# Performance work log

Hardware: AMD Instinct MI355X
Metric: run time of the kernel (lower is better)

## Reference

```python
import jax, jax.numpy as jnp
import numpy as np

B, S, D = 4, 2048, 768
H = 12
DH = D // H  # 64


def setup_inputs() -> dict:
    key = jax.random.key(0)
    ks = jax.random.split(key, 6)
    scale = 0.02
    return {
        "hidden_states": jax.random.normal(ks[0], (B, S, D), dtype=jnp.float32),
        "Wq": jax.random.normal(ks[1], (D, D), dtype=jnp.float32) * scale,
        "bq": jnp.zeros((D,), dtype=jnp.float32),
        "Wk": jax.random.normal(ks[2], (D, D), dtype=jnp.float32) * scale,
        "bk": jnp.zeros((D,), dtype=jnp.float32),
        "Wv": jax.random.normal(ks[3], (D, D), dtype=jnp.float32) * scale,
        "bv": jnp.zeros((D,), dtype=jnp.float32),
        "Wo": jax.random.normal(ks[4], (D, D), dtype=jnp.float32) * scale,
        "bo": jnp.zeros((D,), dtype=jnp.float32),
        "w_mix": jnp.ones((2,), dtype=jnp.float32),
    }


def reference(hidden_states, Wq, bq, Wk, bk, Wv, bv, Wo, bo, w_mix):
    # Q/K/V projections, then split heads: [B,S,D] -> [B,H,S,DH]
    def split_heads(x):
        return x.reshape(B, S, H, DH).transpose(0, 2, 1, 3)

    q = split_heads(hidden_states @ Wq.T + bq)
    k = split_heads(hidden_states @ Wk.T + bk)
    v = split_heads(hidden_states @ Wv.T + bv)

    # [B,H,S,S] attention scores
    scores = jnp.einsum("bhqd,bhkd->bhqk", q, k) / jnp.sqrt(jnp.float32(DH))

    attn_soft = jax.nn.softmax(scores, axis=-1)
    attn_relu2 = jnp.square(jax.nn.relu(scores))
    mix = jax.nn.softmax(w_mix)  # exp(w)/sum(exp(w))
    attn = attn_soft * mix[0] + attn_relu2 * mix[1]
    # dropout rate 0.0 (inference) -> identity

    ctx = jnp.einsum("bhqk,bhkd->bhqd", attn, v)
    ctx = ctx.transpose(0, 2, 1, 3).reshape(B, S, D)
    out = ctx @ Wo.T + bo
    return out
```

## Files before the change

kernel.cpp:

```cpp
#include <hip/hip_runtime.h>

#define DEV __device__ __forceinline__

typedef __attribute__((ext_vector_type(8))) short short8;
typedef __attribute__((ext_vector_type(4))) float f32x4;
typedef __attribute__((ext_vector_type(2))) unsigned int u32x2;
typedef __attribute__((ext_vector_type(4))) unsigned int u32x4;

constexpr int Dm = 768;
constexpr int Sn = 2048;
constexpr int Bn = 4;
constexpr int Hn = 12;
constexpr int Mn = Bn * Sn;

constexpr float kQScale = 0.18033688011112043f;
constexpr float kR2Fix  = 0.4804530139182014f;

DEV unsigned short f32_to_bf16(float f) {
  unsigned int u = __float_as_uint(f);
  u = (u + 0x7fffu + ((u >> 16) & 1u)) >> 16;
  return (unsigned short)u;
}

DEV unsigned cvt_pk_bf16(float lo, float hi) {
  unsigned d;
  asm("v_cvt_pk_bf16_f32 %0, %1, %2" : "=v"(d) : "v"(lo), "v"(hi));
  return d;
}

DEV f32x4 mfma_bf16(short8 a, short8 b, f32x4 c) {
  return __builtin_amdgcn_mfma_f32_16x16x32_bf16(a, b, c, 0, 0, 0);
}

DEV void gload_lds16(const void* g, void* l) {
  __builtin_amdgcn_global_load_lds(
      (__attribute__((address_space(1))) const unsigned int*)g,
      (__attribute__((address_space(3))) unsigned int*)l, 16, 0, 0);
}

DEV short8 transpose_to_bfrag(unsigned xd0, unsigned xd1, unsigned yd0, unsigned yd1) {
  u32x2 a0 = __builtin_amdgcn_permlane32_swap(xd0, yd0, false, false);
  u32x2 b0 = __builtin_amdgcn_permlane16_swap(a0[0], a0[1], false, false);
  u32x2 a1 = __builtin_amdgcn_permlane32_swap(xd1, yd1, false, false);
  u32x2 b1 = __builtin_amdgcn_permlane16_swap(a1[0], a1[1], false, false);
  u32x4 f = {b0[0], b1[0], b0[1], b1[1]};
  return __builtin_bit_cast(short8, f);
}

__global__ __launch_bounds__(256) void k_cast_all(
    const float* __restrict__ hs, const float* __restrict__ Wq,
    const float* __restrict__ Wk, const float* __restrict__ Wv,
    const float* __restrict__ Wo, unsigned short* __restrict__ hbf,
    unsigned short* __restrict__ wbf) {
  int bx = blockIdx.x;
  if (bx < 6144) {
    int i = bx * 256 + threadIdx.x;
    float4 v = ((const float4*)hs)[i];
    ushort4 o;
    o.x = f32_to_bf16(v.x); o.y = f32_to_bf16(v.y);
    o.z = f32_to_bf16(v.z); o.w = f32_to_bf16(v.w);
    ((ushort4*)hbf)[i] = o;
  } else {
    int i = (bx - 6144) * 256 + threadIdx.x;
    int w = i / 147456;
    int off = i - w * 147456;
    const float* src = (w == 0) ? Wq : (w == 1) ? Wk : (w == 2) ? Wv : Wo;
    float4 v = ((const float4*)src)[off];
    ushort4 o;
    o.x = f32_to_bf16(v.x); o.y = f32_to_bf16(v.y);
    o.z = f32_to_bf16(v.z); o.w = f32_to_bf16(v.w);
    ((ushort4*)wbf)[w * 147456 + off] = o;
  }
}

__global__ __launch_bounds__(256, 3) void k_gemm_qkv(
    const unsigned short* __restrict__ Abf, const unsigned short* __restrict__ wbf,
    const float* __restrict__ bq, const float* __restrict__ bk, const float* __restrict__ bv,
    unsigned short* __restrict__ Qb, unsigned short* __restrict__ Kb,
    unsigned short* __restrict__ Vt) {
  __shared__ unsigned short Sh[2 * 10240];

  const int tid = threadIdx.x;
  const int wave = tid >> 6, lane = tid & 63;
  const int wm = wave >> 1, wn = wave & 1;
  const int quad = lane >> 4, l16 = lane & 15;
  const int lin = blockIdx.x;
  const int swz = (lin & 7) * 96 + (lin >> 3);
  const int bxi = swz % 12;
  const int byi = swz / 12;
  const int bm = byi * 128, bn = bxi * 192;
  const int seg = bxi >> 2;
  const int nloc0 = (bxi & 3) * 192;

  const int sr = lane >> 2;
  const int sc = (lane & 3) * 8;
  const unsigned short* gA0 = Abf + (size_t)(bm + (wave * 2 + 0) * 16 + sr) * Dm + sc;
  const unsigned short* gA1 = Abf + (size_t)(bm + (wave * 2 + 1) * 16 + sr) * Dm + sc;
  const unsigned short* gB0 = wbf + (size_t)(bn + (wave * 3 + 0) * 16 + sr) * Dm + sc;
  const unsigned short* gB1 = wbf + (size_t)(bn + (wave * 3 + 1) * 16 + sr) * Dm + sc;
  const unsigned short* gB2 = wbf + (size_t)(bn + (wave * 3 + 2) * 16 + sr) * Dm + sc;
  const int oA0 = (wave * 2 + 0) * 512;
  const int oA1 = (wave * 2 + 1) * 512;
  const int oB0 = 4096 + (wave * 3 + 0) * 512;
  const int oB1 = 4096 + (wave * 3 + 1) * 512;
  const int oB2 = 4096 + (wave * 3 + 2) * 512;

  f32x4 acc[4][6];
#pragma unroll
  for (int i = 0; i < 4; ++i)
#pragma unroll
    for (int j = 0; j < 6; ++j)
#pragma unroll
      for (int r = 0; r < 4; ++r) acc[i][j][r] = 0.f;

  gload_lds16(gA0, &Sh[oA0]);
  gload_lds16(gA1, &Sh[oA1]);
  gload_lds16(gB0, &Sh[oB0]);
  gload_lds16(gB1, &Sh[oB1]);
  gload_lds16(gB2, &Sh[oB2]);
  __syncthreads();

  const unsigned short* pA0 = gA0 + 32;
  const unsigned short* pA1 = gA1 + 32;
  const unsigned short* pB0 = gB0 + 32;
  const unsigned short* pB1 = gB1 + 32;
  const unsigned short* pB2 = gB2 + 32;

  constexpr int NK = Dm / 32;
#pragma unroll 2
  for (int kk = 0; kk < NK; ++kk) {
    const int cur = kk & 1;
    if (kk + 1 < NK) {
      unsigned short* nset = &Sh[(cur ^ 1) * 10240];
      gload_lds16(pA0, nset + oA0);
      gload_lds16(pA1, nset + oA1);
      gload_lds16(pB0, nset + oB0);
      gload_lds16(pB1, nset + oB1);
      gload_lds16(pB2, nset + oB2);
      pA0 += 32; pA1 += 32; pB0 += 32; pB1 += 32; pB2 += 32;
    }

    const unsigned short* As = &Sh[cur * 10240];
    const unsigned short* Bs = As + 4096;
    short8 af[4], bf[6];
#pragma unroll
    for (int mi = 0; mi < 4; ++mi)
      af[mi] = *(const short8*)(&As[(wm * 64 + mi * 16 + l16) * 32 + quad * 8]);
#pragma unroll
    for (int ni = 0; ni < 6; ++ni)
      bf[ni] = *(const short8*)(&Bs[(wn * 96 + ni * 16 + l16) * 32 + quad * 8]);
#pragma unroll
    for (int mi = 0; mi < 4; ++mi)
#pragma unroll
      for (int ni = 0; ni < 6; ++ni)
        acc[mi][ni] = mfma_bf16(af[mi], bf[ni], acc[mi][ni]);
    __syncthreads();
  }

  if (seg != 2) {
    const float* bias = (seg == 0) ? bq : bk;
    unsigned short* Out = (seg == 0) ? Qb : Kb;
    const float scale = (seg == 0) ? kQScale : 1.0f;
#pragma unroll
    for (int ni = 0; ni < 6; ++ni) {
      int n = nloc0 + wn * 96 + ni * 16 + l16;
      float bias_v = bias[n];
#pragma unroll
      for (int mi = 0; mi < 4; ++mi) {
#pragma unroll
        for (int r = 0; r < 4; ++r) {
          int m = bm + wm * 64 + mi * 16 + quad * 4 + r;
          Out[(size_t)m * Dm + n] = f32_to_bf16((acc[mi][ni][r] + bias_v) * scale);
        }
      }
    }
  } else {
    const int bb = bm >> 11;
    const int s0 = bm & 2047;
    const int j = tid >> 4;
    const int cch = tid & 15;
#pragma unroll
    for (int p = 0; p < 2; ++p) {
      if (wn == p) {
#pragma unroll
        for (int ni = 0; ni < 6; ++ni) {
          int nl = ni * 16 + l16;
          float bias_v = bv[nloc0 + p * 96 + nl];
#pragma unroll
          for (int mi = 0; mi < 4; ++mi)
#pragma unroll
            for (int r = 0; r < 4; ++r)
              Sh[nl * 136 + wm * 64 + mi * 16 + quad * 4 + r] =
                  f32_to_bf16(acc[mi][ni][r] + bias_v);
        }
      }
      __syncthreads();
#pragma unroll
      for (int it = 0; it < 6; ++it) {
        int row = it * 16 + j;
        int nv = nloc0 + p * 96 + row;
        int h2 = nv >> 6, dcol = nv & 63;
        uint4 v = *(const uint4*)(&Sh[row * 136 + cch * 8]);
        *(uint4*)(&Vt[((size_t)((bb * Hn + h2) * 64 + dcol)) * Sn + s0 + cch * 8]) = v;
      }
      __syncthreads();
    }
  }
}

__global__ __launch_bounds__(256, 3) void k_attn(
    const unsigned short* __restrict__ Qb, const unsigned short* __restrict__ Kb,
    const unsigned short* __restrict__ Vt, const float* __restrict__ wmix,
    unsigned short* __restrict__ Ctx) {
  __shared__ unsigned short Ks[2][64 * 64];
  __shared__ unsigned short Vs[2][64 * 64];

  const int tid = threadIdx.x;
  const int wave = tid >> 6, lane = tid & 63;
  const int quad = lane >> 4, l16 = lane & 15;
  const int l8 = l16 & 7;
  const int lin = blockIdx.x;
  const int qt = lin / 48;
  const int s = lin % 48;
  const int bh = (s & 7) * 6 + (s >> 3);
  const int b = bh / Hn, h = bh % Hn;

  const unsigned short* Qg = Qb + (size_t)(b * Sn + qt * 128) * Dm + h * 64;
  const unsigned short* Kg = Kb + (size_t)(b * Sn) * Dm + h * 64;
  const unsigned short* Vg = Vt + (size_t)bh * 64 * Sn;

  const int krr = lane >> 3, kcc = lane & 7;
  const int kchunk = kcc ^ krr;

#pragma unroll
  for (int i = 0; i < 4; ++i) {
    int t = wave * 4 + i;
    gload_lds16(Qg + (size_t)(t * 8 + krr) * Dm + kchunk * 8, &Ks[0][0] + t * 512);
  }
  __syncthreads();
  short8 qf[2][2];
#pragma unroll
  for (int mi = 0; mi < 2; ++mi)
#pragma unroll
    for (int ks = 0; ks < 2; ++ks)
      qf[mi][ks] = *(const short8*)(
          &Ks[wave >> 1][((wave & 1) * 32 + mi * 16 + l16) * 64 +
                         (((ks * 4 + quad) ^ l8) << 3)]);
  __syncthreads();

  const f32x4 kZero = {0.f, 0.f, 0.f, 0.f};
  short8 ones;
#pragma unroll
  for (int i = 0; i < 8; ++i) ones[i] = (short)0x3F80;

  f32x4 acc_s[2][4], acc_r2[2][4], lacc[2];
#pragma unroll
  for (int i = 0; i < 2; ++i) {
#pragma unroll
    for (int j = 0; j < 4; ++j)
#pragma unroll
      for (int r = 0; r < 4; ++r) { acc_s[i][j][r] = 0.f; acc_r2[i][j][r] = 0.f; }
#pragma unroll
    for (int r = 0; r < 4; ++r) lacc[i][r] = 0.f;
  }

  const unsigned short* kp0;
  const unsigned short* kp1;
  const unsigned short* vp0;
  const unsigned short* vp1;
  {
    int t0 = wave * 2 + 0, t1 = wave * 2 + 1;
    kp0 = Kg + (size_t)(64 + t0 * 8 + krr) * Dm + kchunk * 8;
    kp1 = Kg + (size_t)(64 + t1 * 8 + krr) * Dm + kchunk * 8;
    vp0 = Vg + (size_t)(t0 * 8 + krr) * Sn + 64 + kchunk * 8;
    vp1 = Vg + (size_t)(t1 * 8 + krr) * Sn + 64 + kchunk * 8;
  }

#pragma unroll
  for (int i = 0; i < 2; ++i) {
    int t = wave * 2 + i;
    gload_lds16(Kg + (size_t)(t * 8 + krr) * Dm + kchunk * 8, &Ks[0][t * 512]);
    gload_lds16(Vg + (size_t)(t * 8 + krr) * Sn + kchunk * 8, &Vs[0][t * 512]);
  }
  __syncthreads();

#pragma unroll 2
  for (int kt = 0; kt < 32; ++kt) {
    const int cur = kt & 1;
    if (kt < 31) {
      const int nxt = cur ^ 1;
      const int t0 = wave * 2 + 0, t1 = wave * 2 + 1;
      gload_lds16(kp0, &Ks[nxt][t0 * 512]);
      gload_lds16(vp0, &Vs[nxt][t0 * 512]);
      gload_lds16(kp1, &Ks[nxt][t1 * 512]);
      gload_lds16(vp1, &Vs[nxt][t1 * 512]);
      kp0 += 64 * Dm; kp1 += 64 * Dm;
      vp0 += 64;      vp1 += 64;
    }

#pragma unroll
    for (int c = 0; c < 2; ++c) {
      short8 kf[2][2];
#pragma unroll
      for (int t2 = 0; t2 < 2; ++t2)
#pragma unroll
        for (int ks = 0; ks < 2; ++ks)
          kf[t2][ks] = *(const short8*)(
              &Ks[cur][(c * 32 + t2 * 16 + l16) * 64 + (((ks * 4 + quad) ^ l8) << 3)]);

      f32x4 sacc[2][2];
      __builtin_amdgcn_s_setprio(1);
#pragma unroll
      for (int mi = 0; mi < 2; ++mi)
#pragma unroll
        for (int t2 = 0; t2 < 2; ++t2)
          sacc[mi][t2] = mfma_bf16(kf[t2][1], qf[mi][1],
                                   mfma_bf16(kf[t2][0], qf[mi][0], kZero));
      __builtin_amdgcn_s_setprio(0);

      short8 vf[4];
#pragma unroll
      for (int nv = 0; nv < 4; ++nv)
        vf[nv] = *(const short8*)(
            &Vs[cur][(nv * 16 + l16) * 64 + (((c * 4 + quad) ^ l8) << 3)]);

#pragma unroll
      for (int mi = 0; mi < 2; ++mi) {
        f32x4 s0 = sacc[mi][0], s1 = sacc[mi][1];
        float p1a[4], p1b[4], p2a[4], p2b[4];
#pragma unroll
        for (int r = 0; r < 4; ++r) {
          p1a[r] = __builtin_amdgcn_exp2f(s0[r]);
          p1b[r] = __builtin_amdgcn_exp2f(s1[r]);
          float t0 = fmaxf(s0[r], 0.f), t1 = fmaxf(s1[r], 0.f);
          p2a[r] = t0 * t0;
          p2b[r] = t1 * t1;
        }
        short8 pf1 = transpose_to_bfrag(cvt_pk_bf16(p1a[0], p1a[1]),
                                        cvt_pk_bf16(p1a[2], p1a[3]),
                                        cvt_pk_bf16(p1b[0], p1b[1]),
                                        cvt_pk_bf16(p1b[2], p1b[3]));
        short8 pf2 = transpose_to_bfrag(cvt_pk_bf16(p2a[0], p2a[1]),
                                        cvt_pk_bf16(p2a[2], p2a[3]),
                                        cvt_pk_bf16(p2b[0], p2b[1]),
                                        cvt_pk_bf16(p2b[2], p2b[3]));
        __builtin_amdgcn_s_setprio(1);
#pragma unroll
        for (int nv = 0; nv < 4; ++nv) {
          acc_s[mi][nv] = mfma_bf16(vf[nv], pf1, acc_s[mi][nv]);
          acc_r2[mi][nv] = mfma_bf16(vf[nv], pf2, acc_r2[mi][nv]);
        }
        lacc[mi] = mfma_bf16(ones, pf1, lacc[mi]);
        __builtin_amdgcn_s_setprio(0);
      }
    }
    __syncthreads();
  }

  float w0 = wmix[0], w1 = wmix[1];
  float e0 = __expf(w0), e1 = __expf(w1);
  float mix0 = e0 / (e0 + e1);
  float mix1 = (e1 / (e0 + e1)) * kR2Fix;

#pragma unroll
  for (int mi = 0; mi < 2; ++mi) {
    float a0 = mix0 / lacc[mi][0];
    int srow = qt * 128 + wave * 32 + mi * 16 + l16;
#pragma unroll
    for (int nv = 0; nv < 4; ++nv) {
      float v0 = fmaf(acc_s[mi][nv][0], a0, mix1 * acc_r2[mi][nv][0]);
      float v1 = fmaf(acc_s[mi][nv][1], a0, mix1 * acc_r2[mi][nv][1]);
      float v2 = fmaf(acc_s[mi][nv][2], a0, mix1 * acc_r2[mi][nv][2]);
      float v3 = fmaf(acc_s[mi][nv][3], a0, mix1 * acc_r2[mi][nv][3]);
      uint2 o;
      o.x = cvt_pk_bf16(v0, v1);
      o.y = cvt_pk_bf16(v2, v3);
      *(uint2*)(&Ctx[(size_t)(b * Sn + srow) * Dm + h * 64 + nv * 16 + quad * 4]) = o;
    }
  }
}

__global__ __launch_bounds__(256, 3) void k_gemm_out(
    const unsigned short* __restrict__ Abf, const unsigned short* __restrict__ W,
    const float* __restrict__ bias, float* __restrict__ out) {
  __shared__ unsigned short Sh2[2 * 8192];

  const int tid = threadIdx.x;
  const int wave = tid >> 6, lane = tid & 63;
  const int wm = wave >> 1, wn = wave & 1;
  const int quad = lane >> 4, l16 = lane & 15;
  const int lin = blockIdx.x;
  const int swz = (lin & 7) * 48 + (lin >> 3);
  const int bxi = swz % 6, byi = swz / 6;
  const int bm = byi * 128, bn = bxi * 128;

  const int sr = lane >> 2;
  const int sc = (lane & 3) * 8;
  const unsigned short* gA0 = Abf + (size_t)(bm + (wave * 2 + 0) * 16 + sr) * Dm + sc;
  const unsigned short* gA1 = Abf + (size_t)(bm + (wave * 2 + 1) * 16 + sr) * Dm + sc;
  const unsigned short* gB0 = W + (size_t)(bn + (wave * 2 + 0) * 16 + sr) * Dm + sc;
  const unsigned short* gB1 = W + (size_t)(bn + (wave * 2 + 1) * 16 + sr) * Dm + sc;
  const int oA0 = (wave * 2 + 0) * 512;
  const int oA1 = (wave * 2 + 1) * 512;
  const int oB0 = 4096 + (wave * 2 + 0) * 512;
  const int oB1 = 4096 + (wave * 2 + 1) * 512;

  f32x4 acc[4][4];
#pragma unroll
  for (int i = 0; i < 4; ++i)
#pragma unroll
    for (int j = 0; j < 4; ++j)
#pragma unroll
      for (int r = 0; r < 4; ++r) acc[i][j][r] = 0.f;

  gload_lds16(gA0, &Sh2[oA0]);
  gload_lds16(gA1, &Sh2[oA1]);
  gload_lds16(gB0, &Sh2[oB0]);
  gload_lds16(gB1, &Sh2[oB1]);
  __syncthreads();

  const unsigned short* pA0 = gA0 + 32;
  const unsigned short* pA1 = gA1 + 32;
  const unsigned short* pB0 = gB0 + 32;
  const unsigned short* pB1 = gB1 + 32;

  constexpr int NK = Dm / 32;
#pragma unroll 2
  for (int kk = 0; kk < NK; ++kk) {
    const int cur = kk & 1;
    if (kk + 1 < NK) {
      unsigned short* nset = &Sh2[(cur ^ 1) * 8192];
      gload_lds16(pA0, nset + oA0);
      gload_lds16(pA1, nset + oA1);
      gload_lds16(pB0, nset + oB0);
      gload_lds16(pB1, nset + oB1);
      pA0 += 32; pA1 += 32; pB0 += 32; pB1 += 32;
    }

    const unsigned short* As = &Sh2[cur * 8192];
    const unsigned short* Bs = As + 4096;
    short8 af[4], bf[4];
#pragma unroll
    for (int mi = 0; mi < 4; ++mi)
      af[mi] = *(const short8*)(&As[(wm * 64 + mi * 16 + l16) * 32 + quad * 8]);
#pragma unroll
    for (int ni = 0; ni < 4; ++ni)
      bf[ni] = *(const short8*)(&Bs[(wn * 64 + ni * 16 + l16) * 32 + quad * 8]);
#pragma unroll
    for (int mi = 0; mi < 4; ++mi)
#pragma unroll
      for (int ni = 0; ni < 4; ++ni)
        acc[mi][ni] = mfma_bf16(af[mi], bf[ni], acc[mi][ni]);
    __syncthreads();
  }

#pragma unroll
  for (int ni = 0; ni < 4; ++ni) {
    int n = bn + wn * 64 + ni * 16 + l16;
    float bias_v = bias[n];
#pragma unroll
    for (int mi = 0; mi < 4; ++mi) {
#pragma unroll
      for (int r = 0; r < 4; ++r) {
        int m = bm + wm * 64 + mi * 16 + quad * 4 + r;
        out[(size_t)m * Dm + n] = acc[mi][ni][r] + bias_v;
      }
    }
  }
}

extern "C" void kernel_launch(void* const* d_in, const int* in_sizes, int n_in,
                              void* d_out, int out_size, void* d_ws, size_t ws_size,
                              hipStream_t stream) {
  const float* hs = (const float*)d_in[0];
  const float* Wq = (const float*)d_in[1];
  const float* bq = (const float*)d_in[2];
  const float* Wk = (const float*)d_in[3];
  const float* bk = (const float*)d_in[4];
  const float* Wv = (const float*)d_in[5];
  const float* bv = (const float*)d_in[6];
  const float* Wo = (const float*)d_in[7];
  const float* bo = (const float*)d_in[8];
  const float* wmix = (const float*)d_in[9];

  unsigned short* hbf = (unsigned short*)d_ws;
  unsigned short* wbf = hbf + (size_t)Mn * Dm;
  unsigned short* Qb  = wbf + (size_t)4 * Dm * Dm;
  unsigned short* Kb  = Qb + (size_t)Mn * Dm;
  unsigned short* Vt  = Kb + (size_t)Mn * Dm;
  unsigned short* Ctx = hbf;

  k_cast_all<<<dim3(8448), dim3(256), 0, stream>>>(hs, Wq, Wk, Wv, Wo, hbf, wbf);
  k_gemm_qkv<<<dim3(768), dim3(256), 0, stream>>>(hbf, wbf, bq, bk, bv, Qb, Kb, Vt);
  k_attn<<<dim3(768), dim3(256), 0, stream>>>(Qb, Kb, Vt, wmix, Ctx);
  k_gemm_out<<<dim3(384), dim3(256), 0, stream>>>(Ctx, wbf + (size_t)3 * Dm * Dm, bo,
                                                  (float*)d_out);
}
```

Before: 230.8 us.

## Fuse hidden-state bf16 cast into QKV GEMM A-tile loading

Removes the separate pass that converts hidden_states to bf16. The QKV GEMM now loads fp32 activations into registers, packs them to bf16 with v_cvt_pk_bf16, and stores them to LDS after the MFMAs for the current stage, which overlaps the conversion with compute. This avoids writing and re-reading a bf16 copy of the activations. In exchange, each activation tile is read 4x over (once per N-block in the segment), now as fp32 at twice the bytes, and the loads go through registers, which raises register pressure under the 3-block occupancy bound.

```diff
diff --git a/kernel.cpp b/kernel.cpp
--- a/kernel.cpp
+++ b/kernel.cpp
@@ -36,6 +36,15 @@
   __builtin_amdgcn_global_load_lds(
       (__attribute__((address_space(1))) const unsigned int*)g,
       (__attribute__((address_space(3))) unsigned int*)l, 16, 0, 0);
+}
+
+DEV uint4 pack8_bf16(float4 a, float4 b) {
+  uint4 o;
+  o.x = cvt_pk_bf16(a.x, a.y);
+  o.y = cvt_pk_bf16(a.z, a.w);
+  o.z = cvt_pk_bf16(b.x, b.y);
+  o.w = cvt_pk_bf16(b.z, b.w);
+  return o;
 }
 
 DEV short8 transpose_to_bfrag(unsigned xd0, unsigned xd1, unsigned yd0, unsigned yd1) {
@@ -47,34 +56,23 @@
   return __builtin_bit_cast(short8, f);
 }
 
-__global__ __launch_bounds__(256) void k_cast_all(
-    const float* __restrict__ hs, const float* __restrict__ Wq,
-    const float* __restrict__ Wk, const float* __restrict__ Wv,
-    const float* __restrict__ Wo, unsigned short* __restrict__ hbf,
+__global__ __launch_bounds__(256) void k_cast_w(
+    const float* __restrict__ Wq, const float* __restrict__ Wk,
+    const float* __restrict__ Wv, const float* __restrict__ Wo,
     unsigned short* __restrict__ wbf) {
-  int bx = blockIdx.x;
-  if (bx < 6144) {
-    int i = bx * 256 + threadIdx.x;
-    float4 v = ((const float4*)hs)[i];
-    ushort4 o;
-    o.x = f32_to_bf16(v.x); o.y = f32_to_bf16(v.y);
-    o.z = f32_to_bf16(v.z); o.w = f32_to_bf16(v.w);
-    ((ushort4*)hbf)[i] = o;
-  } else {
-    int i = (bx - 6144) * 256 + threadIdx.x;
-    int w = i / 147456;
-    int off = i - w * 147456;
-    const float* src = (w == 0) ? Wq : (w == 1) ? Wk : (w == 2) ? Wv : Wo;
-    float4 v = ((const float4*)src)[off];
-    ushort4 o;
-    o.x = f32_to_bf16(v.x); o.y = f32_to_bf16(v.y);
-    o.z = f32_to_bf16(v.z); o.w = f32_to_bf16(v.w);
-    ((ushort4*)wbf)[w * 147456 + off] = o;
-  }
+  int i = blockIdx.x * 256 + threadIdx.x;
+  int w = i / 147456;
+  int off = i - w * 147456;
+  const float* src = (w == 0) ? Wq : (w == 1) ? Wk : (w == 2) ? Wv : Wo;
+  float4 v = ((const float4*)src)[off];
+  ushort4 o;
+  o.x = f32_to_bf16(v.x); o.y = f32_to_bf16(v.y);
+  o.z = f32_to_bf16(v.z); o.w = f32_to_bf16(v.w);
+  ((ushort4*)wbf)[w * 147456 + off] = o;
 }
 
 __global__ __launch_bounds__(256, 3) void k_gemm_qkv(
-    const unsigned short* __restrict__ Abf, const unsigned short* __restrict__ wbf,
+    const float* __restrict__ hs, const unsigned short* __restrict__ wbf,
     const float* __restrict__ bq, const float* __restrict__ bk, const float* __restrict__ bv,
     unsigned short* __restrict__ Qb, unsigned short* __restrict__ Kb,
     unsigned short* __restrict__ Vt) {
@@ -94,13 +92,13 @@
 
   const int sr = lane >> 2;
   const int sc = (lane & 3) * 8;
-  const unsigned short* gA0 = Abf + (size_t)(bm + (wave * 2 + 0) * 16 + sr) * Dm + sc;
-  const unsigned short* gA1 = Abf + (size_t)(bm + (wave * 2 + 1) * 16 + sr) * Dm + sc;
+  const float* gAf0 = hs + (size_t)(bm + (wave * 2 + 0) * 16 + sr) * Dm + sc;
+  const float* gAf1 = hs + (size_t)(bm + (wave * 2 + 1) * 16 + sr) * Dm + sc;
   const unsigned short* gB0 = wbf + (size_t)(bn + (wave * 3 + 0) * 16 + sr) * Dm + sc;
   const unsigned short* gB1 = wbf + (size_t)(bn + (wave * 3 + 1) * 16 + sr) * Dm + sc;
   const unsigned short* gB2 = wbf + (size_t)(bn + (wave * 3 + 2) * 16 + sr) * Dm + sc;
-  const int oA0 = (wave * 2 + 0) * 512;
-  const int oA1 = (wave * 2 + 1) * 512;
+  const int oA0 = (wave * 2 + 0) * 512 + lane * 8;
+  const int oA1 = (wave * 2 + 1) * 512 + lane * 8;
   const int oB0 = 4096 + (wave * 3 + 0) * 512;
   const int oB1 = 4096 + (wave * 3 + 1) * 512;
   const int oB2 = 4096 + (wave * 3 + 2) * 512;
@@ -113,15 +111,21 @@
 #pragma unroll
       for (int r = 0; r < 4; ++r) acc[i][j][r] = 0.f;
 
-  gload_lds16(gA0, &Sh[oA0]);
-  gload_lds16(gA1, &Sh[oA1]);
-  gload_lds16(gB0, &Sh[oB0]);
-  gload_lds16(gB1, &Sh[oB1]);
-  gload_lds16(gB2, &Sh[oB2]);
+  {
+    float4 a00 = *(const float4*)(gAf0);
+    float4 a01 = *(const float4*)(gAf0 + 4);
+    float4 a10 = *(const float4*)(gAf1);
+    float4 a11 = *(const float4*)(gAf1 + 4);
+    gload_lds16(gB0, &Sh[oB0]);
+    gload_lds16(gB1, &Sh[oB1]);
+    gload_lds16(gB2, &Sh[oB2]);
+    *(uint4*)(&Sh[oA0]) = pack8_bf16(a00, a01);
+    *(uint4*)(&Sh[oA1]) = pack8_bf16(a10, a11);
+  }
   __syncthreads();
 
-  const unsigned short* pA0 = gA0 + 32;
-  const unsigned short* pA1 = gA1 + 32;
+  const float* pAf0 = gAf0 + 32;
+  const float* pAf1 = gAf1 + 32;
   const unsigned short* pB0 = gB0 + 32;
   const unsigned short* pB1 = gB1 + 32;
   const unsigned short* pB2 = gB2 + 32;
@@ -130,14 +134,18 @@
 #pragma unroll 2
   for (int kk = 0; kk < NK; ++kk) {
     const int cur = kk & 1;
-    if (kk + 1 < NK) {
-      unsigned short* nset = &Sh[(cur ^ 1) * 10240];
-      gload_lds16(pA0, nset + oA0);
-      gload_lds16(pA1, nset + oA1);
+    float4 a00, a01, a10, a11;
+    unsigned short* nset = &Sh[(cur ^ 1) * 10240];
+    const bool pf = (kk + 1 < NK);
+    if (pf) {
+      a00 = *(const float4*)(pAf0);
+      a01 = *(const float4*)(pAf0 + 4);
+      a10 = *(const float4*)(pAf1);
+      a11 = *(const float4*)(pAf1 + 4);
       gload_lds16(pB0, nset + oB0);
       gload_lds16(pB1, nset + oB1);
       gload_lds16(pB2, nset + oB2);
-      pA0 += 32; pA1 += 32; pB0 += 32; pB1 += 32; pB2 += 32;
+      pAf0 += 32; pAf1 += 32; pB0 += 32; pB1 += 32; pB2 += 32;
     }
 
     const unsigned short* As = &Sh[cur * 10240];
@@ -154,6 +162,11 @@
 #pragma unroll
       for (int ni = 0; ni < 6; ++ni)
         acc[mi][ni] = mfma_bf16(af[mi], bf[ni], acc[mi][ni]);
+
+    if (pf) {
+      *(uint4*)(&nset[oA0]) = pack8_bf16(a00, a01);
+      *(uint4*)(&nset[oA1]) = pack8_bf16(a10, a11);
+    }
     __syncthreads();
   }
 
@@ -490,8 +503,8 @@
   unsigned short* Vt  = Kb + (size_t)Mn * Dm;
   unsigned short* Ctx = hbf;
 
-  k_cast_all<<<dim3(8448), dim3(256), 0, stream>>>(hs, Wq, Wk, Wv, Wo, hbf, wbf);
-  k_gemm_qkv<<<dim3(768), dim3(256), 0, stream>>>(hbf, wbf, bq, bk, bv, Qb, Kb, Vt);
+  k_cast_w<<<dim3(2304), dim3(256), 0, stream>>>(Wq, Wk, Wv, Wo, wbf);
+  k_gemm_qkv<<<dim3(768), dim3(256), 0, stream>>>(hs, wbf, bq, bk, bv, Qb, Kb, Vt);
   k_attn<<<dim3(768), dim3(256), 0, stream>>>(Qb, Kb, Vt, wmix, Ctx);
   k_gemm_out<<<dim3(384), dim3(256), 0, stream>>>(Ctx, wbf + (size_t)3 * Dm * Dm, bo,
                                                   (float*)d_out);
```

After: 232.4 us. No clear change (+0.7%).
